# Kernel optimization log

Measured on AMD Instinct MI355X. Metric: run time of the kernel, lower is better.

The kernel has to match this reference:

```python
import jax, jax.numpy as jnp
import numpy as np

NUM_HEADS = 16
KEEP_RATIO = 0.25
BETA = 1.0
EPS = 1e-6


def setup_inputs() -> dict:
    key = jax.random.key(0)
    ks = jax.random.split(key, 5)
    B, N, C = 16, 577, 1024
    x = jax.random.normal(ks[0], (B, N, C), dtype=jnp.float32)
    qkv_w = jax.random.normal(ks[1], (3 * C, C), dtype=jnp.float32) * (C ** -0.5)
    proj_w = jax.random.normal(ks[2], (C, C), dtype=jnp.float32) * (C ** -0.5)
    proj_b = jax.random.normal(ks[3], (C,), dtype=jnp.float32)
    # visit counts per (head, key); uniform positive
    ucb_count_score = jax.random.uniform(ks[4], (NUM_HEADS, N), dtype=jnp.float32) * 100.0
    return {"x": x, "qkv_w": qkv_w, "proj_w": proj_w, "proj_b": proj_b,
            "ucb_count_score": ucb_count_score, "counter": 100, "ucb_enabled": 1}


def reference(x, qkv_w, proj_w, proj_b, ucb_count_score, counter, ucb_enabled):
    B, N, C = x.shape
    H = NUM_HEADS
    Dh = C // H
    scale = Dh ** -0.5

    qkv = (x @ qkv_w.T).reshape(B, N, 3, H, Dh).transpose(2, 0, 3, 1, 4)  # [3,B,H,N,Dh]
    q, k, v = qkv[0], qkv[1], qkv[2]
    attn_scores = jnp.einsum('bhqd,bhkd->bhqk', q, k) * scale  # [B,H,N,N]

    score_delta = None
    if ucb_enabled and counter > 50:
        # exclude_cls=True: prune only over keys 1..N-1
        nkeys = N - 1
        kk = max(1, int(nkeys * KEEP_RATIO))
        scores_for_topk = attn_scores[..., 1:]                      # [B,H,N,nkeys]
        cnt = ucb_count_score[:, 1:]                                # [H,nkeys]
        expl = BETA * jnp.sqrt(jnp.log(counter + 1.0) / (cnt + EPS))  # [H,nkeys]
        ucb_scores = scores_for_topk + expl[None, :, None, :]
        # top-k mask via flat scatter
        flat = ucb_scores.reshape(-1, nkeys)
        _, top_idx = jax.lax.top_k(flat, kk)                        # [BHN, kk]
        rows = jnp.arange(flat.shape[0])[:, None]
        mask = jnp.zeros(flat.shape, dtype=bool).at[rows, top_idx].set(True)
        mask = mask.reshape(B, H, N, nkeys)
        cls_mask = jnp.ones((B, H, N, 1), dtype=bool)
        mask_full = jnp.concatenate([cls_mask, mask], axis=-1)      # [B,H,N,N]
        neg = -jnp.finfo(attn_scores.dtype).max
        pruned = jnp.where(mask_full, attn_scores, neg)
        attn_probs = jax.nn.softmax(pruned, axis=-1)
        score_delta = mask_full.sum(axis=(0, 2)).astype(jnp.int32)  # [H,N]
    else:
        attn_probs = jax.nn.softmax(attn_scores, axis=-1)

    context = jnp.einsum('bhqk,bhkd->bhqd', attn_probs, v)
    out = context.transpose(0, 2, 1, 3).reshape(B, N, C) @ proj_w.T + proj_b
    return (out, score_delta)
```

## Files before the change

### kernel.cpp

```cpp
#include <hip/hip_runtime.h>
#include <hip/hip_bf16.h>

#define B_ 16
#define N_ 577
#define C_ 1024
#define H_ 16
#define DH_ 64
#define M_ (B_*N_)
#define KKEEP 144
#define VTP 584
#define SST 325

typedef __attribute__((ext_vector_type(8))) short bf16x8;
typedef __attribute__((ext_vector_type(4))) float f32x4;

__device__ __forceinline__ float b2f(unsigned short u){ return __uint_as_float(((unsigned int)u) << 16); }
__device__ __forceinline__ unsigned short f2bu(float f){
  __hip_bfloat16 h = __float2bfloat16(f);
  return *(unsigned short*)&h;
}
__device__ __forceinline__ float wredmaxf(float v){
  #pragma unroll
  for (int m=1;m<64;m<<=1) v = fmaxf(v, __shfl_xor(v, m, 64));
  return v;
}
__device__ __forceinline__ float wredsumf(float v){
  #pragma unroll
  for (int m=1;m<64;m<<=1) v += __shfl_xor(v, m, 64);
  return v;
}

__global__ __launch_bounds__(256) void gemm_qkv_mfma(
    const float* __restrict__ X, const float* __restrict__ W,
    unsigned short* __restrict__ qb, unsigned short* __restrict__ kb,
    unsigned short* __restrict__ vt)
{
  __shared__ unsigned short As[128][40];
  __shared__ unsigned short Bs[128][40];
  const int tid = threadIdx.x;
  const int lane = tid & 63, wave = tid >> 6;
  const int wm = wave >> 1, wn = wave & 1;
  const int lr = lane & 15, kh = lane >> 4;
  const int bm = blockIdx.x*128, bn = blockIdx.y*128;
  const int srow = tid >> 1, shalf = tid & 1;

  f32x4 acc[4][4];
  #pragma unroll
  for (int i=0;i<4;++i)
    #pragma unroll
    for (int j=0;j<4;++j) acc[i][j] = (f32x4){0.f,0.f,0.f,0.f};

  for (int k0=0; k0<1024; k0+=32){
    __syncthreads();
    {
      unsigned short t16[16];
      int m = bm + srow;
      if (m < M_){
        const float4* s = (const float4*)(X + (size_t)m*1024 + k0 + shalf*16);
        #pragma unroll
        for (int g=0; g<4; ++g){
          float4 v = s[g];
          t16[g*4+0]=f2bu(v.x); t16[g*4+1]=f2bu(v.y); t16[g*4+2]=f2bu(v.z); t16[g*4+3]=f2bu(v.w);
        }
      } else {
        #pragma unroll
        for (int g=0; g<16; ++g) t16[g]=0;
      }
      *(uint4*)&As[srow][shalf*16]   = *(uint4*)&t16[0];
      *(uint4*)&As[srow][shalf*16+8] = *(uint4*)&t16[8];

      const float4* sw = (const float4*)(W + (size_t)(bn+srow)*1024 + k0 + shalf*16);
      #pragma unroll
      for (int g=0; g<4; ++g){
        float4 v = sw[g];
        t16[g*4+0]=f2bu(v.x); t16[g*4+1]=f2bu(v.y); t16[g*4+2]=f2bu(v.z); t16[g*4+3]=f2bu(v.w);
      }
      *(uint4*)&Bs[srow][shalf*16]   = *(uint4*)&t16[0];
      *(uint4*)&Bs[srow][shalf*16+8] = *(uint4*)&t16[8];
    }
    __syncthreads();
    bf16x8 af[4], bfr[4];
    #pragma unroll
    for (int f=0; f<4; ++f){
      af[f]  = *(const bf16x8*)&As[wm*64 + f*16 + lr][kh*8];
      bfr[f] = *(const bf16x8*)&Bs[wn*64 + f*16 + lr][kh*8];
    }
    #pragma unroll
    for (int fm=0; fm<4; ++fm)
      #pragma unroll
      for (int fn=0; fn<4; ++fn)
        acc[fm][fn] = __builtin_amdgcn_mfma_f32_16x16x32_bf16(af[fm], bfr[fn], acc[fm][fn], 0,0,0);
  }
  #pragma unroll
  for (int fm=0; fm<4; ++fm){
    #pragma unroll
    for (int j=0; j<4; ++j){
      int m = bm + wm*64 + fm*16 + kh*4 + j;
      if (m >= M_) continue;
      int b = m / N_, n = m - b*N_;
      #pragma unroll
      for (int fn=0; fn<4; ++fn){
        int c = bn + wn*64 + fn*16 + lr;
        int three = c >> 10, hh = (c >> 6) & 15, dd = c & 63;
        unsigned short val = f2bu(acc[fm][fn][j]);
        if (three == 0)      qb[((size_t)(b*H_ + hh)*N_ + n)*DH_ + dd] = val;
        else if (three == 1) kb[((size_t)(b*H_ + hh)*N_ + n)*DH_ + dd] = val;
        else                 vt[((size_t)(b*H_ + hh)*DH_ + dd)*VTP + n] = val;
      }
    }
  }
}

__global__ __launch_bounds__(256,6) void attn_kernel(
    const unsigned short* __restrict__ qw, const unsigned short* __restrict__ kw,
    const unsigned short* __restrict__ vt,
    const float* __restrict__ ucb, const int* __restrict__ counter_p,
    unsigned short* __restrict__ ctx, int* __restrict__ delta)
{
  __shared__ __align__(16) float S[16][SST];
  __shared__ float expl_s[584];
  __shared__ int   cnt_s[584];
  unsigned short (*pus)[584] = (unsigned short (*)[584])&S[0][0];

  const int tid = threadIdx.x;
  const int lane = tid & 63, wave = tid >> 6;
  const int lr = lane & 15, kh = lane >> 4;
  const int blk = blockIdx.x;
  const int bh = blk / 37, tileq = blk % 37;
  const int h = bh & 15;
  const int row0 = tileq * 16;

  const float logc = logf((float)(*counter_p) + 1.0f);
  for (int k2=tid; k2<N_; k2+=256){
    cnt_s[k2] = 0;
    expl_s[k2] = (k2==0) ? 0.f : sqrtf(logc / (ucb[h*N_ + k2] + 1e-6f));
  }

  const unsigned short* qbb = qw + (size_t)bh*N_*DH_;
  const unsigned short* kbb = kw + (size_t)bh*N_*DH_;
  bf16x8 aq0 = {0,0,0,0,0,0,0,0}, aq1 = {0,0,0,0,0,0,0,0};
  {
    int qr = row0 + lr;
    if (qr < N_){
      aq0 = *(const bf16x8*)(qbb + (size_t)qr*DH_ + kh*8);
      aq1 = *(const bf16x8*)(qbb + (size_t)qr*DH_ + 32 + kh*8);
    }
  }

  float acc[4][10];
  #pragma unroll
  for (int r=0;r<4;++r)
    #pragma unroll
    for (int s=0;s<10;++s) acc[r][s]=0.f;

  #pragma unroll
  for (int half=0; half<2; ++half){
    const int t0 = half ? 20 : 0, t1 = half ? 37 : 20, keyoff = half*320;
    for (int tile = t0 + wave; tile < t1; tile += 4){
      int keyr = tile*16 + lr;
      bf16x8 b0 = {0,0,0,0,0,0,0,0}, b1 = {0,0,0,0,0,0,0,0};
      if (keyr < N_){
        b0 = *(const bf16x8*)(kbb + (size_t)keyr*DH_ + kh*8);
        b1 = *(const bf16x8*)(kbb + (size_t)keyr*DH_ + 32 + kh*8);
      }
      f32x4 d = (f32x4){0.f,0.f,0.f,0.f};
      d = __builtin_amdgcn_mfma_f32_16x16x32_bf16(aq0, b0, d, 0,0,0);
      d = __builtin_amdgcn_mfma_f32_16x16x32_bf16(aq1, b1, d, 0,0,0);
      int col = tile*16 - keyoff + lr;
      #pragma unroll
      for (int rg=0; rg<4; ++rg)
        S[kh*4+rg][col] = d[rg];
    }
    __syncthreads();
    #pragma unroll
    for (int s=0; s<5; ++s){
      int sg = half*5 + s;
      int k = sg*64 + lane;
      if (k < N_){
        #pragma unroll
        for (int r=0;r<4;++r) acc[r][sg] = S[wave*4+r][k - keyoff];
      }
    }
    __syncthreads();
  }

  #pragma unroll
  for (int r=0;r<4;++r){
    const int lrow = wave*4 + r;
    const int n = row0 + lrow;
    const bool rv = (n < N_);
    float sc[10], uv[10]; bool vd[10];
    #pragma unroll
    for (int s=0;s<10;++s) sc[s] = acc[r][s]*0.125f;
    float mx0 = -3.4e38f, mn0 = 3.4e38f;
    #pragma unroll
    for (int s=0;s<10;++s){
      int k = s*64 + lane;
      vd[s] = (k >= 1) && (k < N_);
      uv[s] = sc[s] + (k < N_ ? expl_s[k] : 0.f);
      if (vd[s]){ mx0 = fmaxf(mx0, uv[s]); mn0 = fminf(mn0, uv[s]); }
    }
    const float mx1 = wredmaxf(mx0);
    const float mn1 = -wredmaxf(-mn0);
    const float scale = 65534.f / fmaxf(mx1 - mn1, 1e-30f);
    unsigned uq[10];
    #pragma unroll
    for (int s=0;s<10;++s)
      uq[s] = vd[s] ? (1u + (unsigned)((uv[s]-mn1)*scale)) : 0u;

    unsigned T = 0u;
    for (int bit=15; bit>=0; --bit){
      unsigned cand = T | (1u << bit);
      int c = 0;
      #pragma unroll
      for (int s=0;s<10;++s) c += (int)__popcll(__ballot(uq[s] >= cand));
      if (c >= KKEEP) T = cand;
    }
    int cgt = 0;
    #pragma unroll
    for (int s=0;s<10;++s) cgt += (int)__popcll(__ballot(uq[s] > T));
    const int rem = KKEEP - cgt;
    unsigned long long em[10];
    #pragma unroll
    for (int s=0;s<10;++s) em[s] = __ballot(uq[s] == T);
    const unsigned long long below = lane ? (~0ull >> (64 - lane)) : 0ull;
    bool keep[10];
    int pref = 0;
    #pragma unroll
    for (int s=0;s<10;++s){
      int k = s*64 + lane;
      bool kp2 = false;
      if (k == 0) kp2 = true;
      else if (k < N_){
        if (uq[s] > T) kp2 = true;
        else if (uq[s] == T) kp2 = (pref + __popcll(em[s] & below)) < rem;
      }
      keep[s] = kp2;
      pref += __popcll(em[s]);
    }
    float mxs = -3.4e38f;
    #pragma unroll
    for (int s=0;s<10;++s) if (keep[s]) mxs = fmaxf(mxs, sc[s]);
    mxs = wredmaxf(mxs);
    float p[10]; float den = 0.f;
    #pragma unroll
    for (int s=0;s<10;++s){ p[s] = keep[s] ? __expf(sc[s]-mxs) : 0.f; den += p[s]; }
    den = wredsumf(den);
    const float inv = 1.0f/den;
    #pragma unroll
    for (int s=0;s<10;++s){
      int k = s*64 + lane;
      if (k < N_) pus[lrow][k] = f2bu(p[s]*inv);
      if (rv && keep[s]) atomicAdd(&cnt_s[k < N_ ? k : 0], 1);
    }
  }
  __syncthreads();

  {
    const int d0 = wave*16;
    const unsigned short* vtb = vt + ((size_t)bh*DH_ + d0 + lr)*VTP;
    f32x4 od = (f32x4){0.f,0.f,0.f,0.f};
    #pragma unroll 3
    for (int kb2=0; kb2<18; ++kb2){
      bf16x8 pa  = *(const bf16x8*)&pus[lr][kb2*32 + kh*8];
      bf16x8 vb8 = *(const bf16x8*)(vtb + kb2*32 + kh*8);
      od = __builtin_amdgcn_mfma_f32_16x16x32_bf16(pa, vb8, od, 0,0,0);
    }
    const float v576 = b2f(vtb[576]);
    #pragma unroll
    for (int rg=0; rg<4; ++rg){
      int q = kh*4 + rg;
      float o = fmaf(b2f(pus[q][576]), v576, od[rg]);
      int n0 = row0 + q;
      if (n0 < N_) ctx[((size_t)bh*N_ + n0)*DH_ + d0 + lr] = f2bu(o);
    }
  }
  __syncthreads();
  for (int k2=tid; k2<N_; k2+=256){
    int c2 = cnt_s[k2];
    if (c2) atomicAdd(&delta[h*N_ + k2], c2);
  }
}

__global__ __launch_bounds__(256) void gemm_proj_mfma(
    const unsigned short* __restrict__ ctxp, const float* __restrict__ W,
    const float* __restrict__ bias, float* __restrict__ out)
{
  __shared__ unsigned short As[128][40];
  __shared__ unsigned short Bs[128][40];
  const int tid = threadIdx.x;
  const int lane = tid & 63, wave = tid >> 6;
  const int wm = wave >> 1, wn = wave & 1;
  const int lr = lane & 15, kh = lane >> 4;
  const int bm = blockIdx.x*128, bn = blockIdx.y*128;
  const int srow = tid >> 1, shalf = tid & 1;

  f32x4 acc[4][4];
  #pragma unroll
  for (int i=0;i<4;++i)
    #pragma unroll
    for (int j=0;j<4;++j) acc[i][j] = (f32x4){0.f,0.f,0.f,0.f};

  const int m_s = bm + srow;
  const int bb = m_s / N_, nn = m_s - bb*N_;

  for (int k0=0; k0<1024; k0+=32){
    __syncthreads();
    {
      uint4 a0 = {0,0,0,0}, a1 = {0,0,0,0};
      if (m_s < M_){
        int hh = k0 >> 6, dd = (k0 & 63) + shalf*16;
        const uint4* s = (const uint4*)(ctxp + ((size_t)(bb*H_ + hh)*N_ + nn)*DH_ + dd);
        a0 = s[0]; a1 = s[1];
      }
      *(uint4*)&As[srow][shalf*16]   = a0;
      *(uint4*)&As[srow][shalf*16+8] = a1;
      unsigned short t16[16];
      const float4* sw = (const float4*)(W + (size_t)(bn+srow)*1024 + k0 + shalf*16);
      #pragma unroll
      for (int g=0; g<4; ++g){
        float4 v = sw[g];
        t16[g*4+0]=f2bu(v.x); t16[g*4+1]=f2bu(v.y); t16[g*4+2]=f2bu(v.z); t16[g*4+3]=f2bu(v.w);
      }
      *(uint4*)&Bs[srow][shalf*16]   = *(uint4*)&t16[0];
      *(uint4*)&Bs[srow][shalf*16+8] = *(uint4*)&t16[8];
    }
    __syncthreads();
    bf16x8 af[4], bfr[4];
    #pragma unroll
    for (int f=0; f<4; ++f){
      af[f]  = *(const bf16x8*)&As[wm*64 + f*16 + lr][kh*8];
      bfr[f] = *(const bf16x8*)&Bs[wn*64 + f*16 + lr][kh*8];
    }
    #pragma unroll
    for (int fm=0; fm<4; ++fm)
      #pragma unroll
      for (int fn=0; fn<4; ++fn)
        acc[fm][fn] = __builtin_amdgcn_mfma_f32_16x16x32_bf16(af[fm], bfr[fn], acc[fm][fn], 0,0,0);
  }
  float bv[4];
  #pragma unroll
  for (int fn=0; fn<4; ++fn) bv[fn] = bias[bn + wn*64 + fn*16 + lr];
  #pragma unroll
  for (int fm=0; fm<4; ++fm){
    #pragma unroll
    for (int j=0; j<4; ++j){
      int m = bm + wm*64 + fm*16 + kh*4 + j;
      if (m >= M_) continue;
      #pragma unroll
      for (int fn=0; fn<4; ++fn){
        int c = bn + wn*64 + fn*16 + lr;
        out[(size_t)m*1024 + c] = acc[fm][fn][j] + bv[fn];
      }
    }
  }
}

__global__ void delta_to_f32(const int* __restrict__ delta, float* __restrict__ outd){
  int i = blockIdx.x*256 + threadIdx.x;
  if (i < H_*N_) outd[i] = (float)delta[i];
}

extern "C" void kernel_launch(void* const* d_in, const int* in_sizes, int n_in,
                              void* d_out, int out_size, void* d_ws, size_t ws_size,
                              hipStream_t stream) {
  const float* x      = (const float*)d_in[0];
  const float* qkv_w  = (const float*)d_in[1];
  const float* proj_w = (const float*)d_in[2];
  const float* proj_b = (const float*)d_in[3];
  const float* ucb    = (const float*)d_in[4];
  const int*   counter= (const int*)d_in[5];

  float* outO = (float*)d_out;
  float* outD = outO + ((size_t)out_size - (size_t)H_*N_);

  unsigned short* qb = (unsigned short*)d_ws;
  unsigned short* kb = qb + (size_t)M_*C_;
  unsigned short* vt = kb + (size_t)M_*C_;
  int*         delta = (int*)(vt + (size_t)B_*H_*DH_*VTP);

  hipMemsetAsync(delta, 0, (size_t)H_*N_*sizeof(int), stream);
  gemm_qkv_mfma<<<dim3(73,24), 256, 0, stream>>>(x, qkv_w, qb, kb, vt);
  attn_kernel<<<dim3(256*37), 256, 0, stream>>>(qb, kb, vt, ucb, counter, qb , delta);
  gemm_proj_mfma<<<dim3(73,8), 256, 0, stream>>>(qb, proj_w, proj_b, outO);
  delta_to_f32<<<dim3(37), 256, 0, stream>>>(delta, outD);
}
```

Before: 453.8 us.

## Pre-convert inputs to bf16, transpose V separately, and coarsen top-k quantization

Adds a kernel that converts x, qkv_w and proj_w to bf16 once, so both GEMMs load bf16 directly instead of converting fp32 inside every k-step. The QKV GEMM now writes V row-major, and a separate tiled kernel transposes it, replacing the scattered transposed stores. The top-k threshold search quantizes to 10 bits instead of 16, cutting the bisection passes. This adds extra launches and workspace traffic, and the coarser quantization creates more ties at the threshold, which the existing tie-break resolves by index rather than by score, so the selected set may diverge from exact top-k.

New measurement: 378.1 us. 16.7% less time.

```diff
diff --git a/kernel.cpp b/kernel.cpp
--- a/kernel.cpp
+++ b/kernel.cpp
@@ -30,10 +30,25 @@
   return v;
 }
 
+__global__ __launch_bounds__(256) void cvt_bf16(
+    const float* __restrict__ X, const float* __restrict__ Wq, const float* __restrict__ Wp,
+    unsigned short* __restrict__ xb, unsigned short* __restrict__ wqb, unsigned short* __restrict__ wpb)
+{
+  size_t g = (size_t)blockIdx.x*256 + threadIdx.x;
+  const float* src; unsigned short* dst; size_t off;
+  if (g < 1181696){ src = X; dst = xb; off = g*8; }
+  else if (g < 1574912){ src = Wq; dst = wqb; off = (g-1181696)*8; }
+  else { src = Wp; dst = wpb; off = (g-1574912)*8; }
+  float4 a = *(const float4*)(src+off), b = *(const float4*)(src+off+4);
+  unsigned short t[8] = { f2bu(a.x), f2bu(a.y), f2bu(a.z), f2bu(a.w),
+                          f2bu(b.x), f2bu(b.y), f2bu(b.z), f2bu(b.w) };
+  *(uint4*)(dst+off) = *(uint4*)t;
+}
+
 __global__ __launch_bounds__(256) void gemm_qkv_mfma(
-    const float* __restrict__ X, const float* __restrict__ W,
+    const unsigned short* __restrict__ Xb, const unsigned short* __restrict__ Wb,
     unsigned short* __restrict__ qb, unsigned short* __restrict__ kb,
-    unsigned short* __restrict__ vt)
+    unsigned short* __restrict__ vb)
 {
   __shared__ unsigned short As[128][40];
   __shared__ unsigned short Bs[128][40];
@@ -50,33 +65,20 @@
     #pragma unroll
     for (int j=0;j<4;++j) acc[i][j] = (f32x4){0.f,0.f,0.f,0.f};
 
+  const int m_s = bm + srow;
   for (int k0=0; k0<1024; k0+=32){
     __syncthreads();
     {
-      unsigned short t16[16];
-      int m = bm + srow;
-      if (m < M_){
-        const float4* s = (const float4*)(X + (size_t)m*1024 + k0 + shalf*16);
-        #pragma unroll
-        for (int g=0; g<4; ++g){
-          float4 v = s[g];
-          t16[g*4+0]=f2bu(v.x); t16[g*4+1]=f2bu(v.y); t16[g*4+2]=f2bu(v.z); t16[g*4+3]=f2bu(v.w);
-        }
-      } else {
-        #pragma unroll
-        for (int g=0; g<16; ++g) t16[g]=0;
-      }
-      *(uint4*)&As[srow][shalf*16]   = *(uint4*)&t16[0];
-      *(uint4*)&As[srow][shalf*16+8] = *(uint4*)&t16[8];
-
-      const float4* sw = (const float4*)(W + (size_t)(bn+srow)*1024 + k0 + shalf*16);
-      #pragma unroll
-      for (int g=0; g<4; ++g){
-        float4 v = sw[g];
-        t16[g*4+0]=f2bu(v.x); t16[g*4+1]=f2bu(v.y); t16[g*4+2]=f2bu(v.z); t16[g*4+3]=f2bu(v.w);
-      }
-      *(uint4*)&Bs[srow][shalf*16]   = *(uint4*)&t16[0];
-      *(uint4*)&Bs[srow][shalf*16+8] = *(uint4*)&t16[8];
+      uint4 a0={0,0,0,0}, a1={0,0,0,0};
+      if (m_s < M_){
+        const uint4* s = (const uint4*)(Xb + (size_t)m_s*1024 + k0 + shalf*16);
+        a0 = s[0]; a1 = s[1];
+      }
+      *(uint4*)&As[srow][shalf*16]   = a0;
+      *(uint4*)&As[srow][shalf*16+8] = a1;
+      const uint4* sw = (const uint4*)(Wb + (size_t)(bn+srow)*1024 + k0 + shalf*16);
+      *(uint4*)&Bs[srow][shalf*16]   = sw[0];
+      *(uint4*)&Bs[srow][shalf*16+8] = sw[1];
     }
     __syncthreads();
     bf16x8 af[4], bfr[4];
@@ -102,11 +104,46 @@
       for (int fn=0; fn<4; ++fn){
         int c = bn + wn*64 + fn*16 + lr;
         int three = c >> 10, hh = (c >> 6) & 15, dd = c & 63;
+        size_t off = ((size_t)(b*H_ + hh)*N_ + n)*DH_ + dd;
         unsigned short val = f2bu(acc[fm][fn][j]);
-        if (three == 0)      qb[((size_t)(b*H_ + hh)*N_ + n)*DH_ + dd] = val;
-        else if (three == 1) kb[((size_t)(b*H_ + hh)*N_ + n)*DH_ + dd] = val;
-        else                 vt[((size_t)(b*H_ + hh)*DH_ + dd)*VTP + n] = val;
-      }
+        if (three == 0)      qb[off] = val;
+        else if (three == 1) kb[off] = val;
+        else                 vb[off] = val;
+      }
+    }
+  }
+}
+
+__global__ __launch_bounds__(256) void transpose_v(
+    const unsigned short* __restrict__ vb, unsigned short* __restrict__ vt)
+{
+  __shared__ unsigned short tile[64][72];
+  const int t = threadIdx.x;
+  const int bh = blockIdx.x / 10, nt = blockIdx.x % 10;
+  const int n0 = nt*64;
+  {
+    int r = t >> 2, c0 = (t & 3) * 16;
+    int n = n0 + r;
+    uint4 a0={0,0,0,0}, a1={0,0,0,0};
+    if (n < N_){
+      const uint4* s = (const uint4*)(vb + ((size_t)bh*N_ + n)*DH_ + c0);
+      a0 = s[0]; a1 = s[1];
+    }
+    *(uint4*)&tile[r][c0]   = a0;
+    *(uint4*)&tile[r][c0+8] = a1;
+  }
+  __syncthreads();
+  {
+    int d = t & 63, j0 = (t >> 6) * 16;
+    unsigned short v[16];
+    #pragma unroll
+    for (int i=0;i<16;++i) v[i] = tile[j0+i][d];
+    unsigned short* dst = vt + ((size_t)bh*DH_ + d)*VTP + n0 + j0;
+    if (n0 + j0 + 15 <= VTP-1){
+      *(uint4*)dst     = *(uint4*)&v[0];
+      *(uint4*)(dst+8) = *(uint4*)&v[8];
+    } else if (n0 + j0 + 7 <= VTP-1){
+      *(uint4*)dst = *(uint4*)&v[0];
     }
   }
 }
@@ -202,14 +239,14 @@
     }
     const float mx1 = wredmaxf(mx0);
     const float mn1 = -wredmaxf(-mn0);
-    const float scale = 65534.f / fmaxf(mx1 - mn1, 1e-30f);
+    const float scale = 1022.f / fmaxf(mx1 - mn1, 1e-30f);
     unsigned uq[10];
     #pragma unroll
     for (int s=0;s<10;++s)
       uq[s] = vd[s] ? (1u + (unsigned)((uv[s]-mn1)*scale)) : 0u;
 
     unsigned T = 0u;
-    for (int bit=15; bit>=0; --bit){
+    for (int bit=9; bit>=0; --bit){
       unsigned cand = T | (1u << bit);
       int c = 0;
       #pragma unroll
@@ -283,7 +320,7 @@
 }
 
 __global__ __launch_bounds__(256) void gemm_proj_mfma(
-    const unsigned short* __restrict__ ctxp, const float* __restrict__ W,
+    const unsigned short* __restrict__ ctxp, const unsigned short* __restrict__ Wb,
     const float* __restrict__ bias, float* __restrict__ out)
 {
   __shared__ unsigned short As[128][40];
@@ -315,15 +352,9 @@
       }
       *(uint4*)&As[srow][shalf*16]   = a0;
       *(uint4*)&As[srow][shalf*16+8] = a1;
-      unsigned short t16[16];
-      const float4* sw = (const float4*)(W + (size_t)(bn+srow)*1024 + k0 + shalf*16);
-      #pragma unroll
-      for (int g=0; g<4; ++g){
-        float4 v = sw[g];
-        t16[g*4+0]=f2bu(v.x); t16[g*4+1]=f2bu(v.y); t16[g*4+2]=f2bu(v.z); t16[g*4+3]=f2bu(v.w);
-      }
-      *(uint4*)&Bs[srow][shalf*16]   = *(uint4*)&t16[0];
-      *(uint4*)&Bs[srow][shalf*16+8] = *(uint4*)&t16[8];
+      const uint4* sw = (const uint4*)(Wb + (size_t)(bn+srow)*1024 + k0 + shalf*16);
+      *(uint4*)&Bs[srow][shalf*16]   = sw[0];
+      *(uint4*)&Bs[srow][shalf*16+8] = sw[1];
     }
     __syncthreads();
     bf16x8 af[4], bfr[4];
@@ -374,14 +405,20 @@
   float* outO = (float*)d_out;
   float* outD = outO + ((size_t)out_size - (size_t)H_*N_);
 
-  unsigned short* qb = (unsigned short*)d_ws;
-  unsigned short* kb = qb + (size_t)M_*C_;
-  unsigned short* vt = kb + (size_t)M_*C_;
-  int*         delta = (int*)(vt + (size_t)B_*H_*DH_*VTP);
+  unsigned short* xb  = (unsigned short*)d_ws;
+  unsigned short* wqb = xb  + (size_t)M_*C_;
+  unsigned short* wpb = wqb + (size_t)3*C_*C_;
+  unsigned short* qb  = wpb + (size_t)C_*C_;
+  unsigned short* kb  = qb  + (size_t)M_*C_;
+  unsigned short* vb  = kb  + (size_t)M_*C_;
+  unsigned short* vt  = vb  + (size_t)M_*C_;
+  int*         delta  = (int*)(vt + (size_t)B_*H_*DH_*VTP);
 
   hipMemsetAsync(delta, 0, (size_t)H_*N_*sizeof(int), stream);
-  gemm_qkv_mfma<<<dim3(73,24), 256, 0, stream>>>(x, qkv_w, qb, kb, vt);
+  cvt_bf16<<<dim3(6664), 256, 0, stream>>>(x, qkv_w, proj_w, xb, wqb, wpb);
+  gemm_qkv_mfma<<<dim3(73,24), 256, 0, stream>>>(xb, wqb, qb, kb, vb);
+  transpose_v<<<dim3(2560), 256, 0, stream>>>(vb, vt);
   attn_kernel<<<dim3(256*37), 256, 0, stream>>>(qb, kb, vt, ucb, counter, qb , delta);
-  gemm_proj_mfma<<<dim3(73,8), 256, 0, stream>>>(qb, proj_w, proj_b, outO);
+  gemm_proj_mfma<<<dim3(73,8), 256, 0, stream>>>(qb, wpb, proj_b, outO);
   delta_to_f32<<<dim3(37), 256, 0, stream>>>(delta, outD);
 }
```
